# Performance work log

Hardware: AMD Instinct MI355X
Metric: run time of the kernel (lower is better)

Reference implementation:

```python
import jax, jax.numpy as jnp
import numpy as np

FILTER_LENGTH = 800
HOP_LENGTH = 200
WIN_LENGTH = 800
NUM_SAMPLES = 8_000_000


def _make_forward_basis():
    # Real/imag DFT rows (cutoff = N/2+1) times a periodic Hamming window.
    fl, wl = FILTER_LENGTH, WIN_LENGTH
    fourier = np.fft.fft(np.eye(fl))
    cutoff = fl // 2 + 1  # 401
    basis = np.vstack([fourier[:cutoff].real, fourier[:cutoff].imag])  # [802, 800]
    n = np.arange(wl)
    window = 0.54 - 0.46 * np.cos(2.0 * np.pi * n / wl)  # scipy get_window('hamming', wl, fftbins=True)
    basis = basis * window[None, :]
    return jnp.asarray(basis[:, None, :], dtype=jnp.float32)  # [802, 1, 800] (OIH)


def setup_inputs() -> dict:
    key = jax.random.key(0)
    input_data = jax.random.normal(key, (NUM_SAMPLES,), dtype=jnp.float32)
    forward_basis = _make_forward_basis()
    return {"input_data": input_data, "forward_basis": forward_basis}


def reference(input_data, forward_basis):
    fl, hop = FILTER_LENGTH, HOP_LENGTH
    cutoff = fl // 2 + 1
    x = input_data.reshape(1, 1, -1)  # (N=1, C=1, T)
    x = jnp.pad(x, ((0, 0), (0, 0), (fl // 2, fl // 2)), mode='reflect')
    # Strided conv with the dense DFT basis == framed windowed DFT.
    out = jax.lax.conv_general_dilated(
        x, forward_basis, window_strides=(hop,), padding='VALID',
        dimension_numbers=('NCH', 'OIH', 'NCH'))  # [1, 802, n_frames]
    real = out[:, :cutoff, :]
    imag = out[:, cutoff:, :]
    magnitude = jnp.sqrt(real * real + imag * imag)  # [1, 401, n_frames]
    return magnitude
```

## Files before the change

kernel.cpp:

```cpp
#include <hip/hip_runtime.h>


#define FL   800
#define HOP  200
#define CUT  401
#define NS   8000000
#define NT   40001
#define KSTEPS 25

#define FT   64
#define TT   128
#define SLICE_SH 26624
#define XBN  8016000
#define BB_OFF 16032000

typedef short short8 __attribute__((ext_vector_type(8)));
typedef float float4v __attribute__((ext_vector_type(4)));

#define GU32 const __attribute__((address_space(1))) unsigned int*
#define LU32 __attribute__((address_space(3))) unsigned int*

__device__ inline unsigned short f2bf(float f) {
    union { float f; unsigned u; } v; v.f = f;
    unsigned r = v.u + 0x7FFFu + ((v.u >> 16) & 1u);
    return (unsigned short)(r >> 16);
}

__global__ void prep_x(const float* __restrict__ x, short* __restrict__ xb) {
    const int n8 = XBN / 8;
    for (int j = blockIdx.x * blockDim.x + threadIdx.x; j < n8;
         j += gridDim.x * blockDim.x) {
        const int i = j * 8;
        const int s = i - 400;
        short8 o;
        if (s >= 0 && s + 7 < NS) {
            const float4v a = *reinterpret_cast<const float4v*>(x + s);
            const float4v b = *reinterpret_cast<const float4v*>(x + s + 4);
            o[0]=f2bf(a[0]); o[1]=f2bf(a[1]); o[2]=f2bf(a[2]); o[3]=f2bf(a[3]);
            o[4]=f2bf(b[0]); o[5]=f2bf(b[1]); o[6]=f2bf(b[2]); o[7]=f2bf(b[3]);
        } else {
            #pragma unroll
            for (int q = 0; q < 8; ++q) {
                int sq = s + q;
                if (sq < 0) sq = -sq;
                else if (sq >= NS) sq = 2 * NS - 2 - sq;
                o[q] = f2bf(x[sq]);
            }
        }
        *reinterpret_cast<short8*>(xb + i) = o;
    }
}

__global__ void prep_b(const float* __restrict__ basis, short* __restrict__ bb) {
    const int nch = 896 * 100;
    for (int j = blockIdx.x * blockDim.x + threadIdx.x; j < nch;
         j += gridDim.x * blockDim.x) {
        const int row = j / 100;
        const int col = (j % 100) * 8;
        short8 o;
        int src = -1;
        if (row < CUT) src = row;
        else if (row >= 448 && row < 448 + CUT) src = row - 47;
        if (src >= 0) {
            const float* p = basis + (size_t)src * 800 + col;
            const float4v a = *reinterpret_cast<const float4v*>(p);
            const float4v b = *reinterpret_cast<const float4v*>(p + 4);
            o[0]=f2bf(a[0]); o[1]=f2bf(a[1]); o[2]=f2bf(a[2]); o[3]=f2bf(a[3]);
            o[4]=f2bf(b[0]); o[5]=f2bf(b[1]); o[6]=f2bf(b[2]); o[7]=f2bf(b[3]);
        } else {
            #pragma unroll
            for (int q = 0; q < 8; ++q) o[q] = 0;
        }
        *reinterpret_cast<short8*>(bb + (size_t)row * 800 + col) = o;
    }
}

#define MF(A, X, C) C = __builtin_amdgcn_mfma_f32_16x16x32_bf16((A), (X), (C), 0, 0, 0)

#define BODY(KS, FC, FN, NXTBUF, ISSBUF)                                        \
  {                                                                             \
    if ((KS) <= 22) {                                                           \
      __builtin_amdgcn_global_load_lds((GU32)(bsrc0 + ((KS)+2)*32),             \
          (LU32)((ISSBUF) + tid*8), 16, 0, 0);                                  \
      __builtin_amdgcn_global_load_lds((GU32)(bsrc1 + ((KS)+2)*32),             \
          (LU32)((ISSBUF) + 2048 + tid*8), 16, 0, 0);                           \
      asm volatile("s_waitcnt vmcnt(2) lgkmcnt(0)" ::: "memory");               \
    } else {                                                                    \
      asm volatile("s_waitcnt vmcnt(0) lgkmcnt(0)" ::: "memory");               \
    }                                                                           \
    __builtin_amdgcn_s_barrier();                                               \
    asm volatile("" ::: "memory");                                              \
    {                                                                           \
      const short* np_ = (NXTBUF);                                              \
      FN[0] = *reinterpret_cast<const short8*>(np_ + oar0);                     \
      FN[1] = *reinterpret_cast<const short8*>(np_ + oar1);                     \
      FN[2] = *reinterpret_cast<const short8*>(np_ + oai0);                     \
      FN[3] = *reinterpret_cast<const short8*>(np_ + oai1);                     \
      FN[4] = *reinterpret_cast<const short8*>(&sX[xbase + 0*3200 + ((KS)+1)*32]); \
      FN[5] = *reinterpret_cast<const short8*>(&sX[xbase + 1*3200 + ((KS)+1)*32]); \
      FN[6] = *reinterpret_cast<const short8*>(&sX[xbase + 2*3200 + ((KS)+1)*32]); \
      FN[7] = *reinterpret_cast<const short8*>(&sX[xbase + 3*3200 + ((KS)+1)*32]); \
    }                                                                           \
    __builtin_amdgcn_s_setprio(1);                                              \
    MF(FC[0], FC[4], acc_r[0][0]); MF(FC[0], FC[5], acc_r[0][1]);               \
    MF(FC[0], FC[6], acc_r[0][2]); MF(FC[0], FC[7], acc_r[0][3]);               \
    MF(FC[1], FC[4], acc_r[1][0]); MF(FC[1], FC[5], acc_r[1][1]);               \
    MF(FC[1], FC[6], acc_r[1][2]); MF(FC[1], FC[7], acc_r[1][3]);               \
    MF(FC[2], FC[4], acc_i[0][0]); MF(FC[2], FC[5], acc_i[0][1]);               \
    MF(FC[2], FC[6], acc_i[0][2]); MF(FC[2], FC[7], acc_i[0][3]);               \
    MF(FC[3], FC[4], acc_i[1][0]); MF(FC[3], FC[5], acc_i[1][1]);               \
    MF(FC[3], FC[6], acc_i[1][2]); MF(FC[3], FC[7], acc_i[1][3]);               \
    __builtin_amdgcn_s_setprio(0);                                              \
  }

__global__ __launch_bounds__(256, 2)
void stft_mag_kernel(const short* __restrict__ xb,
                     const short* __restrict__ bb,
                     float* __restrict__ out) {
    __shared__ short sX[SLICE_SH];
    __shared__ short sB0[128 * 32];
    __shared__ short sB1[128 * 32];
    __shared__ short sB2[128 * 32];

    const int tid = threadIdx.x;

    const int nwg = 313 * 7;
    const int q = nwg >> 3, r = nwg & 7;
    const int bid = blockIdx.x;
    const int xcd = bid & 7, idx = bid >> 3;
    const int wgid = (xcd < r ? xcd * (q + 1) : r * (q + 1) + (xcd - r) * q) + idx;
    const int t0 = (wgid / 7) * TT;
    const int f0 = (wgid % 7) * FT;

    const int rowc  = tid >> 2;
    const int slot0 = (tid & 3) ^ ((tid >> 3) & 3);
    const short* bsrc0 = bb + (size_t)(f0 + rowc) * 800 + slot0 * 8;
    const short* bsrc1 = bb + (size_t)(448 + f0 + rowc) * 800 + slot0 * 8;

    __builtin_amdgcn_global_load_lds((GU32)(bsrc0), (LU32)(sB0 + tid*8), 16, 0, 0);
    __builtin_amdgcn_global_load_lds((GU32)(bsrc1), (LU32)(sB0 + 2048 + tid*8), 16, 0, 0);
    {
        const short* src = xb + (size_t)t0 * HOP + tid * 8;
        short* dst = sX + tid * 8;
        #pragma unroll
        for (int it = 0; it < 13; ++it) {
            __builtin_amdgcn_global_load_lds((GU32)(src + it * 2048),
                                             (LU32)(dst + it * 2048), 16, 0, 0);
        }
    }
    __builtin_amdgcn_global_load_lds((GU32)(bsrc0 + 32), (LU32)(sB1 + tid*8), 16, 0, 0);
    __builtin_amdgcn_global_load_lds((GU32)(bsrc1 + 32), (LU32)(sB1 + 2048 + tid*8), 16, 0, 0);

    const int wid  = tid >> 6;
    const int lane = tid & 63;
    const int wm   = wid >> 1;
    const int wn   = wid & 1;
    const int l15  = lane & 15;
    const int l4   = lane >> 4;

    const int rr0 = wm * 32 + l15;
    const int rr1 = wm * 32 + 16 + l15;
    const int oar0 = (rr0 * 4 + (l4 ^ ((rr0 >> 1) & 3))) * 8;
    const int oar1 = (rr1 * 4 + (l4 ^ ((rr1 >> 1) & 3))) * 8;
    const int oai0 = ((64 + rr0) * 4 + (l4 ^ (((64 + rr0) >> 1) & 3))) * 8;
    const int oai1 = ((64 + rr1) * 4 + (l4 ^ (((64 + rr1) >> 1) & 3))) * 8;
    const int xbase = (wn * 64 + l15) * HOP + l4 * 8;

    float4v acc_r[2][4] = {};
    float4v acc_i[2][4] = {};

    short8 FA[8], FB[8];

    asm volatile("s_waitcnt vmcnt(2)" ::: "memory");
    __builtin_amdgcn_s_barrier();
    asm volatile("" ::: "memory");
    FA[0] = *reinterpret_cast<const short8*>(sB0 + oar0);
    FA[1] = *reinterpret_cast<const short8*>(sB0 + oar1);
    FA[2] = *reinterpret_cast<const short8*>(sB0 + oai0);
    FA[3] = *reinterpret_cast<const short8*>(sB0 + oai1);
    FA[4] = *reinterpret_cast<const short8*>(&sX[xbase + 0*3200]);
    FA[5] = *reinterpret_cast<const short8*>(&sX[xbase + 1*3200]);
    FA[6] = *reinterpret_cast<const short8*>(&sX[xbase + 2*3200]);
    FA[7] = *reinterpret_cast<const short8*>(&sX[xbase + 3*3200]);

    #pragma unroll
    for (int jj = 0; jj < 24; jj += 6) {
        BODY(jj + 0, FA, FB, sB1, sB2);
        BODY(jj + 1, FB, FA, sB2, sB0);
        BODY(jj + 2, FA, FB, sB0, sB1);
        BODY(jj + 3, FB, FA, sB1, sB2);
        BODY(jj + 4, FA, FB, sB2, sB0);
        BODY(jj + 5, FB, FA, sB0, sB1);
    }

    __builtin_amdgcn_s_setprio(1);
    MF(FA[0], FA[4], acc_r[0][0]); MF(FA[0], FA[5], acc_r[0][1]);
    MF(FA[0], FA[6], acc_r[0][2]); MF(FA[0], FA[7], acc_r[0][3]);
    MF(FA[1], FA[4], acc_r[1][0]); MF(FA[1], FA[5], acc_r[1][1]);
    MF(FA[1], FA[6], acc_r[1][2]); MF(FA[1], FA[7], acc_r[1][3]);
    MF(FA[2], FA[4], acc_i[0][0]); MF(FA[2], FA[5], acc_i[0][1]);
    MF(FA[2], FA[6], acc_i[0][2]); MF(FA[2], FA[7], acc_i[0][3]);
    MF(FA[3], FA[4], acc_i[1][0]); MF(FA[3], FA[5], acc_i[1][1]);
    MF(FA[3], FA[6], acc_i[1][2]); MF(FA[3], FA[7], acc_i[1][3]);
    __builtin_amdgcn_s_setprio(0);

    #pragma unroll
    for (int mi = 0; mi < 2; ++mi) {
        #pragma unroll
        for (int rr = 0; rr < 4; ++rr) {
            const int f = f0 + wm * 32 + mi * 16 + l4 * 4 + rr;
            if (f >= CUT) continue;
            #pragma unroll
            for (int ni = 0; ni < 4; ++ni) {
                const int t = t0 + wn * 64 + ni * 16 + l15;
                if (t < NT) {
                    const float vr = (mi == 0 ? acc_r[0][ni][rr] : acc_r[1][ni][rr]);
                    const float vi = (mi == 0 ? acc_i[0][ni][rr] : acc_i[1][ni][rr]);
                    out[(size_t)f * NT + t] = sqrtf(vr * vr + vi * vi);
                }
            }
        }
    }
}

extern "C" void kernel_launch(void* const* d_in, const int* in_sizes, int n_in,
                              void* d_out, int out_size, void* d_ws, size_t ws_size,
                              hipStream_t stream) {
    const float* x     = (const float*)d_in[0];
    const float* basis = (const float*)d_in[1];
    float* out = (float*)d_out;

    short* xb = (short*)d_ws;
    short* bb = (short*)((char*)d_ws + BB_OFF);

    prep_x<<<2048, 256, 0, stream>>>(x, xb);
    prep_b<<<350, 256, 0, stream>>>(basis, bb);

    stft_mag_kernel<<<313 * 7, 256, 0, stream>>>(xb, bb, out);
}
```

Baseline: 83.72 us.

## Enlarge time tile to 192 and give each wave private basis buffers without barriers

```diff
diff --git a/kernel.cpp b/kernel.cpp
--- a/kernel.cpp
+++ b/kernel.cpp
@@ -9,8 +9,9 @@
 #define KSTEPS 25
 
 #define FT   64
-#define TT   128
-#define SLICE_SH 26624
+#define TT   192
+#define TTILES 209
+#define SLICE_SH 40960
 #define XBN  8016000
 #define BB_OFF 16032000
 
@@ -77,54 +78,57 @@
 
 #define MF(A, X, C) C = __builtin_amdgcn_mfma_f32_16x16x32_bf16((A), (X), (C), 0, 0, 0)
 
-#define BODY(KS, FC, FN, NXTBUF, ISSBUF)                                        \
+#define BODY(KS, FC, FN)                                                        \
   {                                                                             \
     if ((KS) <= 22) {                                                           \
-      __builtin_amdgcn_global_load_lds((GU32)(bsrc0 + ((KS)+2)*32),             \
-          (LU32)((ISSBUF) + tid*8), 16, 0, 0);                                  \
-      __builtin_amdgcn_global_load_lds((GU32)(bsrc1 + ((KS)+2)*32),             \
-          (LU32)((ISSBUF) + 2048 + tid*8), 16, 0, 0);                           \
-      asm volatile("s_waitcnt vmcnt(2) lgkmcnt(0)" ::: "memory");               \
-    } else {                                                                    \
-      asm volatile("s_waitcnt vmcnt(0) lgkmcnt(0)" ::: "memory");               \
+      short* ip_ = sBw + (((KS) + 2) % 3) * 2048 + lane * 8;                    \
+      __builtin_amdgcn_global_load_lds((GU32)(b0 + ((KS)+2)*32), (LU32)(ip_),        16, 0, 0); \
+      __builtin_amdgcn_global_load_lds((GU32)(b1 + ((KS)+2)*32), (LU32)(ip_ + 512),  16, 0, 0); \
+      __builtin_amdgcn_global_load_lds((GU32)(b2 + ((KS)+2)*32), (LU32)(ip_ + 1024), 16, 0, 0); \
+      __builtin_amdgcn_global_load_lds((GU32)(b3 + ((KS)+2)*32), (LU32)(ip_ + 1536), 16, 0, 0); \
+      asm volatile("s_waitcnt vmcnt(4)" ::: "memory");                          \
+    } else if ((KS) == 23) {                                                    \
+      asm volatile("s_waitcnt vmcnt(0)" ::: "memory");                          \
     }                                                                           \
-    __builtin_amdgcn_s_barrier();                                               \
-    asm volatile("" ::: "memory");                                              \
-    {                                                                           \
-      const short* np_ = (NXTBUF);                                              \
-      FN[0] = *reinterpret_cast<const short8*>(np_ + oar0);                     \
-      FN[1] = *reinterpret_cast<const short8*>(np_ + oar1);                     \
-      FN[2] = *reinterpret_cast<const short8*>(np_ + oai0);                     \
-      FN[3] = *reinterpret_cast<const short8*>(np_ + oai1);                     \
+    if ((KS) <= 23) {                                                           \
+      const short* nb_ = sBw + (((KS) + 1) % 3) * 2048;                         \
+      FN[0] = *reinterpret_cast<const short8*>(nb_ + mo0);                      \
+      FN[1] = *reinterpret_cast<const short8*>(nb_ + mo1);                      \
+      FN[2] = *reinterpret_cast<const short8*>(nb_ + mo2);                      \
+      FN[3] = *reinterpret_cast<const short8*>(nb_ + mo3);                      \
       FN[4] = *reinterpret_cast<const short8*>(&sX[xbase + 0*3200 + ((KS)+1)*32]); \
       FN[5] = *reinterpret_cast<const short8*>(&sX[xbase + 1*3200 + ((KS)+1)*32]); \
       FN[6] = *reinterpret_cast<const short8*>(&sX[xbase + 2*3200 + ((KS)+1)*32]); \
       FN[7] = *reinterpret_cast<const short8*>(&sX[xbase + 3*3200 + ((KS)+1)*32]); \
+      FN[8] = *reinterpret_cast<const short8*>(&sX[xbase + 4*3200 + ((KS)+1)*32]); \
+      FN[9] = *reinterpret_cast<const short8*>(&sX[xbase + 5*3200 + ((KS)+1)*32]); \
     }                                                                           \
     __builtin_amdgcn_s_setprio(1);                                              \
     MF(FC[0], FC[4], acc_r[0][0]); MF(FC[0], FC[5], acc_r[0][1]);               \
     MF(FC[0], FC[6], acc_r[0][2]); MF(FC[0], FC[7], acc_r[0][3]);               \
+    MF(FC[0], FC[8], acc_r[0][4]); MF(FC[0], FC[9], acc_r[0][5]);               \
     MF(FC[1], FC[4], acc_r[1][0]); MF(FC[1], FC[5], acc_r[1][1]);               \
     MF(FC[1], FC[6], acc_r[1][2]); MF(FC[1], FC[7], acc_r[1][3]);               \
+    MF(FC[1], FC[8], acc_r[1][4]); MF(FC[1], FC[9], acc_r[1][5]);               \
     MF(FC[2], FC[4], acc_i[0][0]); MF(FC[2], FC[5], acc_i[0][1]);               \
     MF(FC[2], FC[6], acc_i[0][2]); MF(FC[2], FC[7], acc_i[0][3]);               \
+    MF(FC[2], FC[8], acc_i[0][4]); MF(FC[2], FC[9], acc_i[0][5]);               \
     MF(FC[3], FC[4], acc_i[1][0]); MF(FC[3], FC[5], acc_i[1][1]);               \
     MF(FC[3], FC[6], acc_i[1][2]); MF(FC[3], FC[7], acc_i[1][3]);               \
+    MF(FC[3], FC[8], acc_i[1][4]); MF(FC[3], FC[9], acc_i[1][5]);               \
     __builtin_amdgcn_s_setprio(0);                                              \
   }
 
-__global__ __launch_bounds__(256, 2)
+__global__ __launch_bounds__(256, 1)
 void stft_mag_kernel(const short* __restrict__ xb,
                      const short* __restrict__ bb,
                      float* __restrict__ out) {
     __shared__ short sX[SLICE_SH];
-    __shared__ short sB0[128 * 32];
-    __shared__ short sB1[128 * 32];
-    __shared__ short sB2[128 * 32];
+    __shared__ short sB[4 * 3 * 2048];
 
     const int tid = threadIdx.x;
 
-    const int nwg = 313 * 7;
+    const int nwg = TTILES * 7;
     const int q = nwg >> 3, r = nwg & 7;
     const int bid = blockIdx.x;
     const int xcd = bid & 7, idx = bid >> 3;
@@ -132,77 +136,93 @@
     const int t0 = (wgid / 7) * TT;
     const int f0 = (wgid % 7) * FT;
 
-    const int rowc  = tid >> 2;
-    const int slot0 = (tid & 3) ^ ((tid >> 3) & 3);
-    const short* bsrc0 = bb + (size_t)(f0 + rowc) * 800 + slot0 * 8;
-    const short* bsrc1 = bb + (size_t)(448 + f0 + rowc) * 800 + slot0 * 8;
-
-    __builtin_amdgcn_global_load_lds((GU32)(bsrc0), (LU32)(sB0 + tid*8), 16, 0, 0);
-    __builtin_amdgcn_global_load_lds((GU32)(bsrc1), (LU32)(sB0 + 2048 + tid*8), 16, 0, 0);
-    {
-        const short* src = xb + (size_t)t0 * HOP + tid * 8;
-        short* dst = sX + tid * 8;
-        #pragma unroll
-        for (int it = 0; it < 13; ++it) {
-            __builtin_amdgcn_global_load_lds((GU32)(src + it * 2048),
-                                             (LU32)(dst + it * 2048), 16, 0, 0);
-        }
-    }
-    __builtin_amdgcn_global_load_lds((GU32)(bsrc0 + 32), (LU32)(sB1 + tid*8), 16, 0, 0);
-    __builtin_amdgcn_global_load_lds((GU32)(bsrc1 + 32), (LU32)(sB1 + 2048 + tid*8), 16, 0, 0);
-
+    const int lane = tid & 63;
     const int wid  = tid >> 6;
-    const int lane = tid & 63;
     const int wm   = wid >> 1;
     const int wn   = wid & 1;
     const int l15  = lane & 15;
     const int l4   = lane >> 4;
 
-    const int rr0 = wm * 32 + l15;
-    const int rr1 = wm * 32 + 16 + l15;
-    const int oar0 = (rr0 * 4 + (l4 ^ ((rr0 >> 1) & 3))) * 8;
-    const int oar1 = (rr1 * 4 + (l4 ^ ((rr1 >> 1) & 3))) * 8;
-    const int oai0 = ((64 + rr0) * 4 + (l4 ^ (((64 + rr0) >> 1) & 3))) * 8;
-    const int oai1 = ((64 + rr1) * 4 + (l4 ^ (((64 + rr1) >> 1) & 3))) * 8;
-    const int xbase = (wn * 64 + l15) * HOP + l4 * 8;
-
-    float4v acc_r[2][4] = {};
-    float4v acc_i[2][4] = {};
-
-    short8 FA[8], FB[8];
-
-    asm volatile("s_waitcnt vmcnt(2)" ::: "memory");
+    short* sBw = sB + wid * (3 * 2048);
+
+    const short *b0, *b1, *b2, *b3;
+    {
+        const int c0 = lane,      r0_ = c0 >> 2;
+        const int c1 = 64 + lane, r1_ = c1 >> 2;
+        const int c2 = 128 + lane, r2_ = c2 >> 2;
+        const int c3 = 192 + lane, r3_ = c3 >> 2;
+        const int g0 = (r0_ < 32) ? (f0 + wm*32 + r0_) : (448 + f0 + wm*32 + (r0_ - 32));
+        const int g1 = (r1_ < 32) ? (f0 + wm*32 + r1_) : (448 + f0 + wm*32 + (r1_ - 32));
+        const int g2 = (r2_ < 32) ? (f0 + wm*32 + r2_) : (448 + f0 + wm*32 + (r2_ - 32));
+        const int g3 = (r3_ < 32) ? (f0 + wm*32 + r3_) : (448 + f0 + wm*32 + (r3_ - 32));
+        b0 = bb + (size_t)g0 * 800 + ((c0 & 3) ^ ((r0_ >> 1) & 3)) * 8;
+        b1 = bb + (size_t)g1 * 800 + ((c1 & 3) ^ ((r1_ >> 1) & 3)) * 8;
+        b2 = bb + (size_t)g2 * 800 + ((c2 & 3) ^ ((r2_ >> 1) & 3)) * 8;
+        b3 = bb + (size_t)g3 * 800 + ((c3 & 3) ^ ((r3_ >> 1) & 3)) * 8;
+    }
+
+    {
+        short* ip = sBw + lane * 8;
+        __builtin_amdgcn_global_load_lds((GU32)(b0), (LU32)(ip),        16, 0, 0);
+        __builtin_amdgcn_global_load_lds((GU32)(b1), (LU32)(ip + 512),  16, 0, 0);
+        __builtin_amdgcn_global_load_lds((GU32)(b2), (LU32)(ip + 1024), 16, 0, 0);
+        __builtin_amdgcn_global_load_lds((GU32)(b3), (LU32)(ip + 1536), 16, 0, 0);
+    }
+    {
+        const int sx0 = t0 * HOP + tid * 8;
+        short* dst = sX + tid * 8;
+        #pragma unroll
+        for (int it = 0; it < 20; ++it) {
+            int off = sx0 + it * 2048;
+            if (off > XBN - 8) off = XBN - 8;
+            __builtin_amdgcn_global_load_lds((GU32)(xb + off),
+                                             (LU32)(dst + it * 2048), 16, 0, 0);
+        }
+    }
+    {
+        short* ip = sBw + 2048 + lane * 8;
+        __builtin_amdgcn_global_load_lds((GU32)(b0 + 32), (LU32)(ip),        16, 0, 0);
+        __builtin_amdgcn_global_load_lds((GU32)(b1 + 32), (LU32)(ip + 512),  16, 0, 0);
+        __builtin_amdgcn_global_load_lds((GU32)(b2 + 32), (LU32)(ip + 1024), 16, 0, 0);
+        __builtin_amdgcn_global_load_lds((GU32)(b3 + 32), (LU32)(ip + 1536), 16, 0, 0);
+    }
+
+    int mo0, mo1, mo2, mo3;
+    {
+        const int ra = 0  + l15, rb = 16 + l15, rc = 32 + l15, rd = 48 + l15;
+        mo0 = ra * 32 + (l4 ^ ((ra >> 1) & 3)) * 8;
+        mo1 = rb * 32 + (l4 ^ ((rb >> 1) & 3)) * 8;
+        mo2 = rc * 32 + (l4 ^ ((rc >> 1) & 3)) * 8;
+        mo3 = rd * 32 + (l4 ^ ((rd >> 1) & 3)) * 8;
+    }
+    const int xbase = (wn * 96 + l15) * HOP + l4 * 8;
+
+    float4v acc_r[2][6] = {};
+    float4v acc_i[2][6] = {};
+
+    short8 FA[10], FB[10];
+
+    asm volatile("s_waitcnt vmcnt(4)" ::: "memory");
     __builtin_amdgcn_s_barrier();
     asm volatile("" ::: "memory");
-    FA[0] = *reinterpret_cast<const short8*>(sB0 + oar0);
-    FA[1] = *reinterpret_cast<const short8*>(sB0 + oar1);
-    FA[2] = *reinterpret_cast<const short8*>(sB0 + oai0);
-    FA[3] = *reinterpret_cast<const short8*>(sB0 + oai1);
+
+    FA[0] = *reinterpret_cast<const short8*>(sBw + mo0);
+    FA[1] = *reinterpret_cast<const short8*>(sBw + mo1);
+    FA[2] = *reinterpret_cast<const short8*>(sBw + mo2);
+    FA[3] = *reinterpret_cast<const short8*>(sBw + mo3);
     FA[4] = *reinterpret_cast<const short8*>(&sX[xbase + 0*3200]);
     FA[5] = *reinterpret_cast<const short8*>(&sX[xbase + 1*3200]);
     FA[6] = *reinterpret_cast<const short8*>(&sX[xbase + 2*3200]);
     FA[7] = *reinterpret_cast<const short8*>(&sX[xbase + 3*3200]);
+    FA[8] = *reinterpret_cast<const short8*>(&sX[xbase + 4*3200]);
+    FA[9] = *reinterpret_cast<const short8*>(&sX[xbase + 5*3200]);
 
     #pragma unroll
-    for (int jj = 0; jj < 24; jj += 6) {
-        BODY(jj + 0, FA, FB, sB1, sB2);
-        BODY(jj + 1, FB, FA, sB2, sB0);
-        BODY(jj + 2, FA, FB, sB0, sB1);
-        BODY(jj + 3, FB, FA, sB1, sB2);
-        BODY(jj + 4, FA, FB, sB2, sB0);
-        BODY(jj + 5, FB, FA, sB0, sB1);
-    }
-
-    __builtin_amdgcn_s_setprio(1);
-    MF(FA[0], FA[4], acc_r[0][0]); MF(FA[0], FA[5], acc_r[0][1]);
-    MF(FA[0], FA[6], acc_r[0][2]); MF(FA[0], FA[7], acc_r[0][3]);
-    MF(FA[1], FA[4], acc_r[1][0]); MF(FA[1], FA[5], acc_r[1][1]);
-    MF(FA[1], FA[6], acc_r[1][2]); MF(FA[1], FA[7], acc_r[1][3]);
-    MF(FA[2], FA[4], acc_i[0][0]); MF(FA[2], FA[5], acc_i[0][1]);
-    MF(FA[2], FA[6], acc_i[0][2]); MF(FA[2], FA[7], acc_i[0][3]);
-    MF(FA[3], FA[4], acc_i[1][0]); MF(FA[3], FA[5], acc_i[1][1]);
-    MF(FA[3], FA[6], acc_i[1][2]); MF(FA[3], FA[7], acc_i[1][3]);
-    __builtin_amdgcn_s_setprio(0);
+    for (int j = 0; j < 12; ++j) {
+        BODY(2*j,     FA, FB);
+        BODY(2*j + 1, FB, FA);
+    }
+    BODY(24, FA, FB);
 
     #pragma unroll
     for (int mi = 0; mi < 2; ++mi) {
@@ -211,8 +231,8 @@
             const int f = f0 + wm * 32 + mi * 16 + l4 * 4 + rr;
             if (f >= CUT) continue;
             #pragma unroll
-            for (int ni = 0; ni < 4; ++ni) {
-                const int t = t0 + wn * 64 + ni * 16 + l15;
+            for (int ni = 0; ni < 6; ++ni) {
+                const int t = t0 + wn * 96 + ni * 16 + l15;
                 if (t < NT) {
                     const float vr = (mi == 0 ? acc_r[0][ni][rr] : acc_r[1][ni][rr]);
                     const float vi = (mi == 0 ? acc_i[0][ni][rr] : acc_i[1][ni][rr]);
@@ -236,5 +256,5 @@
     prep_x<<<2048, 256, 0, stream>>>(x, xb);
     prep_b<<<350, 256, 0, stream>>>(basis, bb);
 
-    stft_mag_kernel<<<313 * 7, 256, 0, stream>>>(xb, bb, out);
-}
+    stft_mag_kernel<<<TTILES * 7, 256, 0, stream>>>(xb, bb, out);
+}
```

Measured after the change: 97.98 us. 17.0% more time.
